# Kernel tuning notes

Hardware: AMD Instinct MI355X
Metric: run time of the kernel (lower is better)

Reference implementation:

```python
import jax, jax.numpy as jnp
import numpy as np
import math

D_INNER = 512
D_STATE = 16
DT_RANK = 32
B_SZ = 2
L_SEQ = 4096


def setup_inputs() -> dict:
    key = jax.random.key(0)
    ks = jax.random.split(key, 6)
    x = jax.random.normal(ks[0], (B_SZ, L_SEQ, D_INNER), dtype=jnp.float32)
    # parameters (match torch init semantics closely enough for a numeric baseline)
    A = jnp.arange(1, D_STATE + 1, dtype=jnp.float32)
    A_log = jnp.broadcast_to(jnp.log(A)[None, :], (D_INNER, D_STATE)).copy()
    D_param = jnp.ones((D_INNER,), dtype=jnp.float32)
    # x_proj: Linear(d_inner -> dt_rank + 2*d_state), no bias
    W_xproj = jax.random.normal(ks[1], (DT_RANK + 2 * D_STATE, D_INNER), dtype=jnp.float32) / np.sqrt(D_INNER)
    # dt_proj: Linear(dt_rank -> d_inner) with special bias init
    W_dt = jax.random.normal(ks[2], (D_INNER, DT_RANK), dtype=jnp.float32) / np.sqrt(DT_RANK)
    dt_init = jnp.exp(jax.random.uniform(ks[3], (D_INNER,)) * (math.log(0.1) - math.log(0.001)) + math.log(0.001))
    b_dt = jnp.log(jnp.exp(dt_init) - 1.0)
    alpha = jnp.asarray(0.6, dtype=jnp.float32)
    beta_logit = jnp.asarray(math.log(0.99 / (1.0 - 0.99 + 1e-08)), dtype=jnp.float32)
    return {"x": x, "A_log": A_log, "D_param": D_param, "W_xproj": W_xproj,
            "W_dt": W_dt, "b_dt": b_dt, "alpha": alpha, "beta_logit": beta_logit}


def _momentum_ssm(x, A_log, D_param, W_xproj, W_dt, b_dt, alpha, beta_logit):
    # x: (B, L, D)
    proj = jnp.einsum('bld,pd->blp', x, W_xproj)            # (B, L, r+2N)
    dt_in = proj[..., :DT_RANK]
    Bp = proj[..., DT_RANK:DT_RANK + D_STATE]                # (B, L, N)
    Cp = proj[..., DT_RANK + D_STATE:]                       # (B, L, N)
    dt = jax.nn.softplus(jnp.einsum('blr,dr->bld', dt_in, W_dt) + b_dt)  # (B, L, D)
    A = -jnp.exp(A_log)                                      # (D, N)
    A_bar = jnp.exp(dt[..., None] * A[None, None])           # (B, L, D, N)
    # fused B_bar * x_t: dt * Bp * x
    inp = dt[..., None] * Bp[:, :, None, :] * x[..., None]   # (B, L, D, N)
    beta = jax.nn.sigmoid(beta_logit)

    # scan over time; carry (h, v): (B, D, N)
    h0 = jnp.zeros((x.shape[0], D_INNER, D_STATE), dtype=x.dtype)
    v0 = jnp.zeros_like(h0)

    def step(carry, ts):
        h, v = carry
        a_t, inp_t, c_t = ts                                 # (B,D,N), (B,D,N), (B,N)
        v = beta * v + alpha * inp_t
        h = a_t * h + v
        y = jnp.einsum('bdn,bn->bd', h, c_t)
        return (h, v), y

    xs = (jnp.moveaxis(A_bar, 1, 0), jnp.moveaxis(inp, 1, 0), jnp.moveaxis(Cp, 1, 0))
    _, ys = jax.lax.scan(step, (h0, v0), xs)                 # ys: (L, B, D)
    y = jnp.moveaxis(ys, 0, 1)                               # (B, L, D)
    return y + D_param * x


def reference(x, A_log, D_param, W_xproj, W_dt, b_dt, alpha, beta_logit):
    return _momentum_ssm(x, A_log, D_param, W_xproj, W_dt, b_dt, alpha, beta_logit)
```

## Files before the change

### kernel.cpp

```cpp
#include <hip/hip_runtime.h>


#define D_IN 512
#define D_ST 16
#define DTR  32
#define BSZ  2
#define LSEQ 4096
#define PDIM 64
#define NCH  256
#define LCH  (LSEQ / NCH)
#define LOG2E 1.44269504f
#define LN2   0.69314718f

typedef __attribute__((ext_vector_type(8))) short short8;
typedef __attribute__((ext_vector_type(4))) float f32x4;

__device__ inline float fast_exp2(float x) { return __builtin_amdgcn_exp2f(x); }
__device__ inline float fast_log2(float x) { return __builtin_amdgcn_logf(x); }

__device__ inline unsigned short bf16_rne(float f) {
  unsigned b = __float_as_uint(f);
  return (unsigned short)((b + 0x7fffu + ((b >> 16) & 1u)) >> 16);
}

__device__ inline void cvt8(const float4 u, const float4 v, short8& hi, short8& lo) {
  float f[8] = {u.x, u.y, u.z, u.w, v.x, v.y, v.z, v.w};
#pragma unroll
  for (int i = 0; i < 8; ++i) {
    unsigned short h = bf16_rne(f[i]);
    hi[i] = (short)h;
    float r = f[i] - __uint_as_float((unsigned)h << 16);
    lo[i] = (short)bf16_rne(r);
  }
}

__global__ __launch_bounds__(256) void k_wprep(const float* __restrict__ W,
                                               short* __restrict__ Whi,
                                               short* __restrict__ Wlo) {
  const int i = (blockIdx.x * 256 + threadIdx.x) * 4;
  float4 w = *(const float4*)(W + i);
  float f[4] = {w.x, w.y, w.z, w.w};
  unsigned short h[4], lo[4];
#pragma unroll
  for (int j = 0; j < 4; ++j) {
    h[j] = bf16_rne(f[j]);
    float r = f[j] - __uint_as_float((unsigned)h[j] << 16);
    lo[j] = bf16_rne(r);
  }
  *(uint2*)(Whi + i) = make_uint2(h[0] | ((unsigned)h[1] << 16), h[2] | ((unsigned)h[3] << 16));
  *(uint2*)(Wlo + i) = make_uint2(lo[0] | ((unsigned)lo[1] << 16), lo[2] | ((unsigned)lo[3] << 16));
}

#define MM3(ACC, AH, AL, BH, BL)                                        \
  ACC = __builtin_amdgcn_mfma_f32_16x16x32_bf16(AL, BH, ACC, 0, 0, 0);  \
  ACC = __builtin_amdgcn_mfma_f32_16x16x32_bf16(AH, BL, ACC, 0, 0, 0);  \
  ACC = __builtin_amdgcn_mfma_f32_16x16x32_bf16(AH, BH, ACC, 0, 0, 0);

#define LOADB(P, S)                                   \
  {                                                   \
    const int kb = ((S) & 15) * 32;                   \
    P##h0 = *(const short8*)(bh + kb);                \
    P##h1 = *(const short8*)(bh + 8192 + kb);         \
    P##h2 = *(const short8*)(bh + 16384 + kb);        \
    P##h3 = *(const short8*)(bh + 24576 + kb);        \
    P##l0 = *(const short8*)(bl + kb);                \
    P##l1 = *(const short8*)(bl + 8192 + kb);         \
    P##l2 = *(const short8*)(bl + 16384 + kb);        \
    P##l3 = *(const short8*)(bl + 24576 + kb);        \
  }

#define LOADA(Aa, Ab, S)                              \
  {                                                   \
    const int ka = ((S) & 15) * 32;                   \
    Aa = *(const float4*)(xr + ka);                   \
    Ab = *(const float4*)(xr + ka + 4);               \
  }

#define SUBSTEP(Aa, Ab, P, SA, SB)                    \
  {                                                   \
    short8 ahi, alo;                                  \
    cvt8(Aa, Ab, ahi, alo);                           \
    MM3(acc0, ahi, alo, P##h0, P##l0);                \
    MM3(acc1, ahi, alo, P##h1, P##l1);                \
    MM3(acc2, ahi, alo, P##h2, P##l2);                \
    MM3(acc3, ahi, alo, P##h3, P##l3);                \
    LOADB(P, SB);                                     \
    LOADA(Aa, Ab, SA);                                \
  }

__global__ __launch_bounds__(64) void k_proj(const float* __restrict__ x,
                                             const short* __restrict__ Whi,
                                             const short* __restrict__ Wlo,
                                             float* __restrict__ proj) {
  const int row0 = blockIdx.x * 16;
  const int l = threadIdx.x;
  const int m = l & 15;
  const int ko = (l >> 4) * 8;
  const float* xr = x + (size_t)(row0 + m) * D_IN + ko;
  const short* bh = Whi + (size_t)m * D_IN + ko;
  const short* bl = Wlo + (size_t)m * D_IN + ko;

  f32x4 acc0 = {0.f, 0.f, 0.f, 0.f}, acc1 = acc0, acc2 = acc0, acc3 = acc0;
  float4 A0a, A0b, A1a, A1b, A2a, A2b, A3a, A3b;
  short8 Xh0, Xh1, Xh2, Xh3, Xl0, Xl1, Xl2, Xl3;
  short8 Yh0, Yh1, Yh2, Yh3, Yl0, Yl1, Yl2, Yl3;
  LOADA(A0a, A0b, 0); LOADA(A1a, A1b, 1); LOADA(A2a, A2b, 2); LOADA(A3a, A3b, 3);
  LOADB(X, 0); LOADB(Y, 1);

#pragma unroll
  for (int it = 0; it < 4; ++it) {
    const int s = it * 4;
    SUBSTEP(A0a, A0b, X, s + 4, s + 2);
    SUBSTEP(A1a, A1b, Y, s + 5, s + 3);
    SUBSTEP(A2a, A2b, X, s + 6, s + 4);
    SUBSTEP(A3a, A3b, Y, s + 7, s + 5);
  }

  const int r0 = (l >> 4) * 4;
#pragma unroll
  for (int r = 0; r < 4; ++r) {
    float* pr = proj + (size_t)(row0 + r0 + r) * PDIM + m;
    pr[0] = acc0[r]; pr[16] = acc1[r]; pr[32] = acc2[r]; pr[48] = acc3[r];
  }
}

__global__ __launch_bounds__(256) void k_scan1(const float* __restrict__ x,
                                               const float* __restrict__ proj,
                                               const float* __restrict__ A_log,
                                               const float* __restrict__ W_dt,
                                               const float* __restrict__ b_dt,
                                               const float* __restrict__ alpha_p,
                                               const float* __restrict__ beta_p,
                                               float* __restrict__ hh,
                                               float* __restrict__ vh,
                                               float* __restrict__ cvv,
                                               float* __restrict__ sdt,
                                               float2* __restrict__ dtx) {
  __shared__ float Ps[LCH][PDIM];
  const int c = blockIdx.x, b = blockIdx.z;
  const int d = blockIdx.y * 256 + threadIdx.x;
  const int t0 = c * LCH;
  {
    const float4* src = (const float4*)(proj + ((size_t)b * LSEQ + t0) * PDIM);
    ((float4*)&Ps[0][0])[threadIdx.x] = src[threadIdx.x];
  }
  float xs[LCH];
  {
    const float* xp = x + ((size_t)b * LSEQ + t0) * D_IN + d;
#pragma unroll
    for (int j = 0; j < LCH; ++j) xs[j] = xp[(size_t)j * D_IN];
  }
  const float alpha = alpha_p[0];
  const float beta = 1.f / (1.f + __expf(-beta_p[0]));
  float A2[D_ST];
  {
    const float4* ap = (const float4*)(A_log + (size_t)d * D_ST);
#pragma unroll
    for (int i = 0; i < 4; ++i) {
      float4 a4 = ap[i];
      A2[4 * i + 0] = -__expf(a4.x) * LOG2E;
      A2[4 * i + 1] = -__expf(a4.y) * LOG2E;
      A2[4 * i + 2] = -__expf(a4.z) * LOG2E;
      A2[4 * i + 3] = -__expf(a4.w) * LOG2E;
    }
  }
  __syncthreads();

  float dtv[LCH];
  {
    float4 w4[8];
    const float4* wp = (const float4*)(W_dt + (size_t)d * DTR);
#pragma unroll
    for (int i = 0; i < 8; ++i) w4[i] = wp[i];
    const float bb = b_dt[d];
#pragma unroll
    for (int j = 0; j < LCH; ++j) {
      const float4* pj = (const float4*)&Ps[j][0];
      float a0 = bb, a1 = 0.f, a2 = 0.f, a3 = 0.f;
#pragma unroll
      for (int k = 0; k < 8; ++k) {
        float4 p = pj[k];
        a0 = fmaf(p.x, w4[k].x, a0);
        a1 = fmaf(p.y, w4[k].y, a1);
        a2 = fmaf(p.z, w4[k].z, a2);
        a3 = fmaf(p.w, w4[k].w, a3);
      }
      float acc = (a0 + a1) + (a2 + a3);
      float e = fast_exp2(acc * LOG2E);
      dtv[j] = (acc > 20.f) ? acc : LN2 * fast_log2(1.f + e);
    }
  }
  {
    float2* dp = dtx + ((size_t)b * LSEQ + t0) * D_IN + d;
#pragma unroll
    for (int j = 0; j < LCH; ++j) dp[(size_t)j * D_IN] = make_float2(dtv[j], xs[j]);
  }

  float h[16] = {}, v[16] = {}, cv[16] = {};
  float bpow = 1.f, sd = 0.f;
#pragma unroll
  for (int j = 0; j < LCH; ++j) {
    const float dtc = dtv[j], xv = xs[j];
    sd += dtc;
    bpow *= beta;
    const float u = alpha * dtc * xv;
    float4 Bq[4];
#pragma unroll
    for (int i = 0; i < 4; ++i) Bq[i] = ((const float4*)&Ps[j][DTR])[i];
    const float* Bf = (const float*)Bq;
#pragma unroll
    for (int n = 0; n < 16; ++n) {
      float a = fast_exp2(dtc * A2[n]);
      v[n] = fmaf(beta, v[n], u * Bf[n]);
      h[n] = fmaf(a, h[n], v[n]);
      cv[n] = fmaf(a, cv[n], bpow);
    }
  }

  const size_t base = ((size_t)(b * NCH + c) * D_IN + d) * D_ST;
#pragma unroll
  for (int i = 0; i < 4; ++i) {
    *(float4*)(hh + base + 4 * i) = ((float4*)h)[i];
    *(float4*)(vh + base + 4 * i) = ((float4*)v)[i];
    *(float4*)(cvv + base + 4 * i) = ((float4*)cv)[i];
  }
  sdt[(size_t)(b * NCH + c) * D_IN + d] = sd;
}

__global__ __launch_bounds__(64) void k_fix(float* __restrict__ hh,
                                            float* __restrict__ vh,
                                            const float* __restrict__ cvv,
                                            const float* __restrict__ sdt,
                                            const float* __restrict__ A_log,
                                            const float* __restrict__ beta_p) {
  const int g = blockIdx.x * 64 + threadIdx.x;
  const int b = g >> 13;
  const int dn = g & 8191;
  const float beta = 1.f / (1.f + __expf(-beta_p[0]));
  const float A2 = -__expf(A_log[dn]) * LOG2E;
  float bL = beta;
#pragma unroll
  for (int i = 0; i < 4; ++i) bL *= bL;

  const size_t cs = (size_t)D_IN * D_ST;
  const size_t base = (size_t)b * NCH * cs + dn;
  const size_t sbase = (size_t)b * NCH * D_IN + (dn >> 4);

  float hg[8], vg[8], cg[8], sg[8];
#pragma unroll
  for (int i = 0; i < 8; ++i) {
    hg[i] = hh[base + i * cs];
    vg[i] = vh[base + i * cs];
    cg[i] = cvv[base + i * cs];
    sg[i] = sdt[sbase + i * D_IN];
  }
  float H = 0.f, V = 0.f;
  for (int c0 = 0; c0 < NCH; c0 += 8) {
    const int cp = (c0 + 8) & (NCH - 1);
    float hn[8], vn[8], cn[8], sn[8];
#pragma unroll
    for (int i = 0; i < 8; ++i) {
      hn[i] = hh[base + (size_t)(cp + i) * cs];
      vn[i] = vh[base + (size_t)(cp + i) * cs];
      cn[i] = cvv[base + (size_t)(cp + i) * cs];
      sn[i] = sdt[sbase + (size_t)(cp + i) * D_IN];
    }
#pragma unroll
    for (int i = 0; i < 8; ++i) {
      hh[base + (size_t)(c0 + i) * cs] = H;
      vh[base + (size_t)(c0 + i) * cs] = V;
      const float Pa = fast_exp2(sg[i] * A2);
      const float Hn = fmaf(Pa, H, fmaf(cg[i], V, hg[i]));
      V = fmaf(bL, V, vg[i]);
      H = Hn;
    }
#pragma unroll
    for (int i = 0; i < 8; ++i) { hg[i] = hn[i]; vg[i] = vn[i]; cg[i] = cn[i]; sg[i] = sn[i]; }
  }
}

__global__ __launch_bounds__(256) void k_scan2(const float2* __restrict__ dtx,
                                               const float* __restrict__ proj,
                                               const float* __restrict__ A_log,
                                               const float* __restrict__ D_param,
                                               const float* __restrict__ alpha_p,
                                               const float* __restrict__ beta_p,
                                               const float* __restrict__ hh,
                                               const float* __restrict__ vh,
                                               float* __restrict__ out) {
  __shared__ float Ps[LCH][PDIM];
  const int c = blockIdx.x, b = blockIdx.z;
  const int d = blockIdx.y * 256 + threadIdx.x;
  const int t0 = c * LCH;
  {
    const float4* src = (const float4*)(proj + ((size_t)b * LSEQ + t0) * PDIM);
    ((float4*)&Ps[0][0])[threadIdx.x] = src[threadIdx.x];
  }
  float2 dx[LCH];
  {
    const float2* dp = dtx + ((size_t)b * LSEQ + t0) * D_IN + d;
#pragma unroll
    for (int j = 0; j < LCH; ++j) dx[j] = dp[(size_t)j * D_IN];
  }
  const float alpha = alpha_p[0];
  const float beta = 1.f / (1.f + __expf(-beta_p[0]));
  const float Dv = D_param[d];
  float A2[D_ST];
  {
    const float4* ap = (const float4*)(A_log + (size_t)d * D_ST);
#pragma unroll
    for (int i = 0; i < 4; ++i) {
      float4 a4 = ap[i];
      A2[4 * i + 0] = -__expf(a4.x) * LOG2E;
      A2[4 * i + 1] = -__expf(a4.y) * LOG2E;
      A2[4 * i + 2] = -__expf(a4.z) * LOG2E;
      A2[4 * i + 3] = -__expf(a4.w) * LOG2E;
    }
  }
  const size_t ibase = ((size_t)(b * NCH + c) * D_IN + d) * D_ST;
  float h[16], v[16];
#pragma unroll
  for (int i = 0; i < 4; ++i) {
    ((float4*)h)[i] = *(const float4*)(hh + ibase + 4 * i);
    ((float4*)v)[i] = *(const float4*)(vh + ibase + 4 * i);
  }
  __syncthreads();

  float* op = out + ((size_t)b * LSEQ + t0) * D_IN + d;
#pragma unroll
  for (int j = 0; j < LCH; ++j) {
    const float dtc = dx[j].x, xv = dx[j].y;
    const float u = alpha * dtc * xv;
    float4 Bq[8];
#pragma unroll
    for (int i = 0; i < 8; ++i) Bq[i] = ((const float4*)&Ps[j][DTR])[i];
    const float* Bf = (const float*)Bq;
    float y0 = 0.f, y1 = 0.f, y2 = 0.f, y3 = 0.f;
#pragma unroll
    for (int n = 0; n < 16; ++n) {
      float a = fast_exp2(dtc * A2[n]);
      v[n] = fmaf(beta, v[n], u * Bf[n]);
      h[n] = fmaf(a, h[n], v[n]);
      float hc = h[n] * Bf[16 + n];
      if ((n & 3) == 0) y0 += hc;
      else if ((n & 3) == 1) y1 += hc;
      else if ((n & 3) == 2) y2 += hc;
      else y3 += hc;
    }
    op[(size_t)j * D_IN] = (y0 + y1) + (y2 + y3) + Dv * xv;
  }
}

extern "C" void kernel_launch(void* const* d_in, const int* in_sizes, int n_in,
                              void* d_out, int out_size, void* d_ws, size_t ws_size,
                              hipStream_t stream) {
  const float* x = (const float*)d_in[0];
  const float* A_log = (const float*)d_in[1];
  const float* D_param = (const float*)d_in[2];
  const float* W_xproj = (const float*)d_in[3];
  const float* W_dt = (const float*)d_in[4];
  const float* b_dt = (const float*)d_in[5];
  const float* alpha = (const float*)d_in[6];
  const float* beta_logit = (const float*)d_in[7];
  float* out = (float*)d_out;

  float* ws = (float*)d_ws;
  float* proj = ws;
  float* hh = proj + (size_t)BSZ * LSEQ * PDIM;
  float* vh = hh + (size_t)BSZ * NCH * D_IN * D_ST;
  float* cvv = vh + (size_t)BSZ * NCH * D_IN * D_ST;
  float* sdt = cvv + (size_t)BSZ * NCH * D_IN * D_ST;
  float2* dtx = (float2*)(sdt + (size_t)BSZ * NCH * D_IN);
  short* Whi = (short*)(dtx + (size_t)BSZ * LSEQ * D_IN);
  short* Wlo = Whi + (size_t)PDIM * D_IN;

  k_wprep<<<dim3(PDIM * D_IN / 1024), dim3(256), 0, stream>>>(W_xproj, Whi, Wlo);
  k_proj<<<dim3(BSZ * LSEQ / 16), dim3(64), 0, stream>>>(x, Whi, Wlo, proj);
  k_scan1<<<dim3(NCH, D_IN / 256, BSZ), dim3(256), 0, stream>>>(
      x, proj, A_log, W_dt, b_dt, alpha, beta_logit, hh, vh, cvv, sdt, dtx);
  k_fix<<<dim3(BSZ * D_IN * D_ST / 64), dim3(64), 0, stream>>>(hh, vh, cvv, sdt, A_log,
                                                               beta_logit);
  k_scan2<<<dim3(NCH, D_IN / 256, BSZ), dim3(256), 0, stream>>>(
      dtx, proj, A_log, D_param, alpha, beta_logit, hh, vh, out);
}
```

Baseline: 181.1 us.

## Store chunk scan states and dt intermediates in fp16, reread x directly

The per-chunk h, v and decay-carry state buffers and the dt intermediate move from fp32 to fp16. The packed (dt, x) float2 buffer is dropped, so scan2 rereads x from the original input. This roughly halves intermediate global-memory traffic across scan1, fix and scan2. The trade is reduced precision in the carried states and dt, which could push error past tolerance, especially for dt feeding exp.

```diff
diff --git a/kernel.cpp b/kernel.cpp
--- a/kernel.cpp
+++ b/kernel.cpp
@@ -14,6 +14,8 @@
 
 typedef __attribute__((ext_vector_type(8))) short short8;
 typedef __attribute__((ext_vector_type(4))) float f32x4;
+typedef _Float16 f16;
+typedef __attribute__((ext_vector_type(8))) _Float16 f16x8;
 
 __device__ inline float fast_exp2(float x) { return __builtin_amdgcn_exp2f(x); }
 __device__ inline float fast_log2(float x) { return __builtin_amdgcn_logf(x); }
@@ -32,6 +34,20 @@
     float r = f[i] - __uint_as_float((unsigned)h << 16);
     lo[i] = (short)bf16_rne(r);
   }
+}
+
+__device__ inline void st16h(f16* p, const float* s) {
+  f16 t[16];
+#pragma unroll
+  for (int i = 0; i < 16; ++i) t[i] = (f16)s[i];
+  *(f16x8*)p = *(f16x8*)&t[0];
+  *(f16x8*)(p + 8) = *(f16x8*)&t[8];
+}
+__device__ inline void ld16h(const f16* p, float* d) {
+  f16x8 a = *(const f16x8*)p;
+  f16x8 b = *(const f16x8*)(p + 8);
+#pragma unroll
+  for (int i = 0; i < 8; ++i) { d[i] = (float)a[i]; d[8 + i] = (float)b[i]; }
 }
 
 __global__ __launch_bounds__(256) void k_wprep(const float* __restrict__ W,
@@ -131,11 +147,11 @@
                                                const float* __restrict__ b_dt,
                                                const float* __restrict__ alpha_p,
                                                const float* __restrict__ beta_p,
-                                               float* __restrict__ hh,
-                                               float* __restrict__ vh,
-                                               float* __restrict__ cvv,
+                                               f16* __restrict__ hh,
+                                               f16* __restrict__ vh,
+                                               f16* __restrict__ cvv,
                                                float* __restrict__ sdt,
-                                               float2* __restrict__ dtx) {
+                                               f16* __restrict__ dth) {
   __shared__ float Ps[LCH][PDIM];
   const int c = blockIdx.x, b = blockIdx.z;
   const int d = blockIdx.y * 256 + threadIdx.x;
@@ -191,9 +207,9 @@
     }
   }
   {
-    float2* dp = dtx + ((size_t)b * LSEQ + t0) * D_IN + d;
-#pragma unroll
-    for (int j = 0; j < LCH; ++j) dp[(size_t)j * D_IN] = make_float2(dtv[j], xs[j]);
+    f16* dp = dth + ((size_t)b * LSEQ + t0) * D_IN + d;
+#pragma unroll
+    for (int j = 0; j < LCH; ++j) dp[(size_t)j * D_IN] = (f16)dtv[j];
   }
 
   float h[16] = {}, v[16] = {}, cv[16] = {};
@@ -218,18 +234,15 @@
   }
 
   const size_t base = ((size_t)(b * NCH + c) * D_IN + d) * D_ST;
-#pragma unroll
-  for (int i = 0; i < 4; ++i) {
-    *(float4*)(hh + base + 4 * i) = ((float4*)h)[i];
-    *(float4*)(vh + base + 4 * i) = ((float4*)v)[i];
-    *(float4*)(cvv + base + 4 * i) = ((float4*)cv)[i];
-  }
+  st16h(hh + base, h);
+  st16h(vh + base, v);
+  st16h(cvv + base, cv);
   sdt[(size_t)(b * NCH + c) * D_IN + d] = sd;
 }
 
-__global__ __launch_bounds__(64) void k_fix(float* __restrict__ hh,
-                                            float* __restrict__ vh,
-                                            const float* __restrict__ cvv,
+__global__ __launch_bounds__(64) void k_fix(f16* __restrict__ hh,
+                                            f16* __restrict__ vh,
+                                            const f16* __restrict__ cvv,
                                             const float* __restrict__ sdt,
                                             const float* __restrict__ A_log,
                                             const float* __restrict__ beta_p) {
@@ -249,9 +262,9 @@
   float hg[8], vg[8], cg[8], sg[8];
 #pragma unroll
   for (int i = 0; i < 8; ++i) {
-    hg[i] = hh[base + i * cs];
-    vg[i] = vh[base + i * cs];
-    cg[i] = cvv[base + i * cs];
+    hg[i] = (float)hh[base + i * cs];
+    vg[i] = (float)vh[base + i * cs];
+    cg[i] = (float)cvv[base + i * cs];
     sg[i] = sdt[sbase + i * D_IN];
   }
   float H = 0.f, V = 0.f;
@@ -260,15 +273,15 @@
     float hn[8], vn[8], cn[8], sn[8];
 #pragma unroll
     for (int i = 0; i < 8; ++i) {
-      hn[i] = hh[base + (size_t)(cp + i) * cs];
-      vn[i] = vh[base + (size_t)(cp + i) * cs];
-      cn[i] = cvv[base + (size_t)(cp + i) * cs];
+      hn[i] = (float)hh[base + (size_t)(cp + i) * cs];
+      vn[i] = (float)vh[base + (size_t)(cp + i) * cs];
+      cn[i] = (float)cvv[base + (size_t)(cp + i) * cs];
       sn[i] = sdt[sbase + (size_t)(cp + i) * D_IN];
     }
 #pragma unroll
     for (int i = 0; i < 8; ++i) {
-      hh[base + (size_t)(c0 + i) * cs] = H;
-      vh[base + (size_t)(c0 + i) * cs] = V;
+      hh[base + (size_t)(c0 + i) * cs] = (f16)H;
+      vh[base + (size_t)(c0 + i) * cs] = (f16)V;
       const float Pa = fast_exp2(sg[i] * A2);
       const float Hn = fmaf(Pa, H, fmaf(cg[i], V, hg[i]));
       V = fmaf(bL, V, vg[i]);
@@ -279,14 +292,15 @@
   }
 }
 
-__global__ __launch_bounds__(256) void k_scan2(const float2* __restrict__ dtx,
+__global__ __launch_bounds__(256) void k_scan2(const float* __restrict__ x,
+                                               const f16* __restrict__ dth,
                                                const float* __restrict__ proj,
                                                const float* __restrict__ A_log,
                                                const float* __restrict__ D_param,
                                                const float* __restrict__ alpha_p,
                                                const float* __restrict__ beta_p,
-                                               const float* __restrict__ hh,
-                                               const float* __restrict__ vh,
+                                               const f16* __restrict__ hh,
+                                               const f16* __restrict__ vh,
                                                float* __restrict__ out) {
   __shared__ float Ps[LCH][PDIM];
   const int c = blockIdx.x, b = blockIdx.z;
@@ -296,11 +310,14 @@
     const float4* src = (const float4*)(proj + ((size_t)b * LSEQ + t0) * PDIM);
     ((float4*)&Ps[0][0])[threadIdx.x] = src[threadIdx.x];
   }
-  float2 dx[LCH];
-  {
-    const float2* dp = dtx + ((size_t)b * LSEQ + t0) * D_IN + d;
-#pragma unroll
-    for (int j = 0; j < LCH; ++j) dx[j] = dp[(size_t)j * D_IN];
+  float xs[LCH], dtv[LCH];
+  {
+    const float* xp = x + ((size_t)b * LSEQ + t0) * D_IN + d;
+    const f16* dp = dth + ((size_t)b * LSEQ + t0) * D_IN + d;
+#pragma unroll
+    for (int j = 0; j < LCH; ++j) xs[j] = xp[(size_t)j * D_IN];
+#pragma unroll
+    for (int j = 0; j < LCH; ++j) dtv[j] = (float)dp[(size_t)j * D_IN];
   }
   const float alpha = alpha_p[0];
   const float beta = 1.f / (1.f + __expf(-beta_p[0]));
@@ -319,17 +336,14 @@
   }
   const size_t ibase = ((size_t)(b * NCH + c) * D_IN + d) * D_ST;
   float h[16], v[16];
-#pragma unroll
-  for (int i = 0; i < 4; ++i) {
-    ((float4*)h)[i] = *(const float4*)(hh + ibase + 4 * i);
-    ((float4*)v)[i] = *(const float4*)(vh + ibase + 4 * i);
-  }
+  ld16h(hh + ibase, h);
+  ld16h(vh + ibase, v);
   __syncthreads();
 
   float* op = out + ((size_t)b * LSEQ + t0) * D_IN + d;
 #pragma unroll
   for (int j = 0; j < LCH; ++j) {
-    const float dtc = dx[j].x, xv = dx[j].y;
+    const float dtc = dtv[j], xv = xs[j];
     const float u = alpha * dtc * xv;
     float4 Bq[8];
 #pragma unroll
@@ -364,22 +378,23 @@
   const float* beta_logit = (const float*)d_in[7];
   float* out = (float*)d_out;
 
+  const size_t NST = (size_t)BSZ * NCH * D_IN * D_ST;
   float* ws = (float*)d_ws;
   float* proj = ws;
-  float* hh = proj + (size_t)BSZ * LSEQ * PDIM;
-  float* vh = hh + (size_t)BSZ * NCH * D_IN * D_ST;
-  float* cvv = vh + (size_t)BSZ * NCH * D_IN * D_ST;
-  float* sdt = cvv + (size_t)BSZ * NCH * D_IN * D_ST;
-  float2* dtx = (float2*)(sdt + (size_t)BSZ * NCH * D_IN);
-  short* Whi = (short*)(dtx + (size_t)BSZ * LSEQ * D_IN);
+  float* sdt = proj + (size_t)BSZ * LSEQ * PDIM;
+  f16* hh = (f16*)(sdt + (size_t)BSZ * NCH * D_IN);
+  f16* vh = hh + NST;
+  f16* cvv = vh + NST;
+  f16* dth = cvv + NST;
+  short* Whi = (short*)(dth + (size_t)BSZ * LSEQ * D_IN);
   short* Wlo = Whi + (size_t)PDIM * D_IN;
 
   k_wprep<<<dim3(PDIM * D_IN / 1024), dim3(256), 0, stream>>>(W_xproj, Whi, Wlo);
   k_proj<<<dim3(BSZ * LSEQ / 16), dim3(64), 0, stream>>>(x, Whi, Wlo, proj);
   k_scan1<<<dim3(NCH, D_IN / 256, BSZ), dim3(256), 0, stream>>>(
-      x, proj, A_log, W_dt, b_dt, alpha, beta_logit, hh, vh, cvv, sdt, dtx);
+      x, proj, A_log, W_dt, b_dt, alpha, beta_logit, hh, vh, cvv, sdt, dth);
   k_fix<<<dim3(BSZ * D_IN * D_ST / 64), dim3(64), 0, stream>>>(hh, vh, cvv, sdt, A_log,
                                                                beta_logit);
   k_scan2<<<dim3(NCH, D_IN / 256, BSZ), dim3(256), 0, stream>>>(
-      dtx, proj, A_log, D_param, alpha, beta_logit, hh, vh, out);
-}
+      x, dth, proj, A_log, D_param, alpha, beta_logit, hh, vh, out);
+}
```

Measured after the change: 174.1 us. 1.04x faster.
